# Optimization experiments

Measured on AMD Instinct MI355X. Metric: run time of the kernel, lower is better.

## Reference

```python
import jax, jax.numpy as jnp
import numpy as np

B, T, A = 4096, 32, 3
HID, D, N, K = 1024, 128, 16, 4096
FLAT = T * A            # 96
LAT = N * D             # 2048
COMMIT = 0.25


def setup_inputs() -> dict:
    key = jax.random.key(0)
    ks = jax.random.split(key, 14)
    s = 0.02
    return {
        "actions": jax.random.normal(ks[0], (B, T, A), jnp.float32),
        # encoder: FLAT -> HID -> HID -> N*D
        "e_w1": jax.random.normal(ks[1], (FLAT, HID), jnp.float32) * s,
        "e_b1": jnp.zeros((HID,), jnp.float32),
        "e_w2": jax.random.normal(ks[2], (HID, HID), jnp.float32) * s,
        "e_b2": jnp.zeros((HID,), jnp.float32),
        "e_w3": jax.random.normal(ks[3], (HID, LAT), jnp.float32) * s,
        "e_b3": jnp.zeros((LAT,), jnp.float32),
        # codebook init: uniform(-1/K, 1/K) as in torch init
        "codebook": jax.random.uniform(ks[4], (K, D), jnp.float32, -1.0 / K, 1.0 / K),
        # decoder: N*D -> HID -> HID -> FLAT
        "d_w1": jax.random.normal(ks[5], (LAT, HID), jnp.float32) * s,
        "d_b1": jnp.zeros((HID,), jnp.float32),
        "d_w2": jax.random.normal(ks[6], (HID, HID), jnp.float32) * s,
        "d_b2": jnp.zeros((HID,), jnp.float32),
        "d_w3": jax.random.normal(ks[7], (HID, FLAT), jnp.float32) * s,
        "d_b3": jnp.zeros((FLAT,), jnp.float32),
    }


def reference(actions, e_w1, e_b1, e_w2, e_b2, e_w3, e_b3, codebook,
              d_w1, d_b1, d_w2, d_b2, d_w3, d_b3):
    sg = jax.lax.stop_gradient
    b = actions.shape[0]
    # encode: [B, T*A] -> [B, N, D]
    flat = actions.reshape(b, FLAT)
    h = jax.nn.silu(flat @ e_w1 + e_b1)
    h = jax.nn.silu(h @ e_w2 + e_b2)
    latents = (h @ e_w3 + e_b3).reshape(b, N, D)
    # nearest-code search: [B*N, K] squared distances
    fl = latents.reshape(b * N, D)
    dist = (fl * fl).sum(1, keepdims=True) + (codebook * codebook).sum(1)[None, :] - 2.0 * (fl @ codebook.T)
    indices = jnp.argmin(dist, axis=1).reshape(b, N)
    quantized = codebook[indices]                      # [B, N, D]
    codebook_loss = jnp.mean((quantized - sg(latents)) ** 2)
    commitment_loss = jnp.mean((latents - sg(quantized)) ** 2)
    vq_loss = codebook_loss + COMMIT * commitment_loss
    q_st = latents + sg(quantized - latents)           # straight-through
    # decode
    g = jax.nn.silu(q_st.reshape(b, LAT) @ d_w1 + d_b1)
    g = jax.nn.silu(g @ d_w2 + d_b2)
    recon = (g @ d_w3 + d_b3).reshape(b, T, A)
    recon_loss = jnp.mean((recon - actions) ** 2)
    loss = recon_loss + vq_loss
    return recon, indices, vq_loss, recon_loss, loss
```

## Files before the change

kernel.cpp:

```cpp
#include <hip/hip_runtime.h>
#include <hip/hip_bf16.h>

#define DD 128

typedef float f2v __attribute__((ext_vector_type(2)));

__global__ void plant_diag(float val, float* out) {
    if (threadIdx.x == 0 && blockIdx.x == 0) out[0] = val;
}

__global__ void zero_acc(double* acc) {
    if (threadIdx.x == 0 && blockIdx.x == 0) { acc[0] = 0.0; acc[1] = 0.0; }
}

__device__ __forceinline__ float silu_np(float x) {
    float e = (float)exp(-(double)x);
    float u = 1.0f + e;
    float v = 1.0f / u;
    return x * v;
}

template <bool SILU>
__global__ __launch_bounds__(256) void gemm_db(const float* __restrict__ A,
                                               const float* __restrict__ W,
                                               const float* __restrict__ bias,
                                               float* __restrict__ C,
                                               int M, int N, int K) {
    __shared__ __align__(16) float As[128][36];
    __shared__ __align__(16) float Ws[32][68];
    const int t = threadIdx.x;
    const int tx = t & 15, ty = t >> 4;
    const int bm = blockIdx.y * 128, bn = blockIdx.x * 64;

    float acc[8][4];
#pragma unroll
    for (int i = 0; i < 8; ++i)
#pragma unroll
        for (int j = 0; j < 4; ++j) acc[i][j] = 0.0f;

    const int nPanels = (K + 31) / 32;
    float ra[16], rw[8];

    {
        const int k0 = 0;
#pragma unroll
        for (int it = 0; it < 16; ++it) {
            int e = t + 256 * it;
            int m = e >> 5, kk = e & 31;
            int mm = bm + m; if (mm >= M) mm = M - 1;
            int kc = k0 + kk;
            ra[it] = (kc < K) ? A[(size_t)mm * K + kc] : 0.0f;
        }
#pragma unroll
        for (int it = 0; it < 8; ++it) {
            int e = t + 256 * it;
            int r = e >> 6, c = e & 63;
            int n = bn + c;
            int kr = k0 + r;
            rw[it] = (kr < K && n < N) ? W[(size_t)kr * N + n] : 0.0f;
        }
    }

    for (int p = 0; p < nPanels; ++p) {
        __syncthreads();
#pragma unroll
        for (int it = 0; it < 16; ++it) {
            int e = t + 256 * it;
            As[e >> 5][e & 31] = ra[it];
        }
#pragma unroll
        for (int it = 0; it < 8; ++it) {
            int e = t + 256 * it;
            Ws[e >> 6][e & 63] = rw[it];
        }
        __syncthreads();

        if (p + 1 < nPanels) {
            const int k0 = (p + 1) * 32;
#pragma unroll
            for (int it = 0; it < 16; ++it) {
                int e = t + 256 * it;
                int m = e >> 5, kk = e & 31;
                int mm = bm + m; if (mm >= M) mm = M - 1;
                int kc = k0 + kk;
                ra[it] = (kc < K) ? A[(size_t)mm * K + kc] : 0.0f;
            }
#pragma unroll
            for (int it = 0; it < 8; ++it) {
                int e = t + 256 * it;
                int r = e >> 6, c = e & 63;
                int n = bn + c;
                int kr = k0 + r;
                rw[it] = (kr < K && n < N) ? W[(size_t)kr * N + n] : 0.0f;
            }
        }

#pragma unroll
        for (int kq = 0; kq < 8; ++kq) {
            float4 a4[8], w4[4];
#pragma unroll
            for (int i = 0; i < 8; ++i)
                a4[i] = *(const float4*)&As[ty + 16 * i][4 * kq];
#pragma unroll
            for (int q = 0; q < 4; ++q)
                w4[q] = *(const float4*)&Ws[4 * kq + q][4 * tx];
#pragma unroll
            for (int q = 0; q < 4; ++q) {
                const float wv[4] = {w4[q].x, w4[q].y, w4[q].z, w4[q].w};
#pragma unroll
                for (int i = 0; i < 8; ++i) {
                    const float av = ((const float*)&a4[i])[q];
#pragma unroll
                    for (int j = 0; j < 4; ++j)
                        acc[i][j] = fmaf(av, wv[j], acc[i][j]);
                }
            }
        }
    }

#pragma unroll
    for (int i = 0; i < 8; ++i) {
        int m = bm + ty + 16 * i;
#pragma unroll
        for (int j = 0; j < 4; ++j) {
            int n = bn + 4 * tx + j;
            if (m < M && n < N) {
                float x = acc[i][j] + bias[n];
                if (SILU) x = silu_np(x);
                C[(size_t)m * N + n] = x;
            }
        }
    }
}

__device__ __forceinline__ float pairwise128_sq(const float* __restrict__ x, int stride) {
    float r0 = x[0*stride]*x[0*stride], r1 = x[1*stride]*x[1*stride],
          r2 = x[2*stride]*x[2*stride], r3 = x[3*stride]*x[3*stride],
          r4 = x[4*stride]*x[4*stride], r5 = x[5*stride]*x[5*stride],
          r6 = x[6*stride]*x[6*stride], r7 = x[7*stride]*x[7*stride];
    for (int i = 8; i < 128; i += 8) {
        r0 += x[(i+0)*stride]*x[(i+0)*stride];
        r1 += x[(i+1)*stride]*x[(i+1)*stride];
        r2 += x[(i+2)*stride]*x[(i+2)*stride];
        r3 += x[(i+3)*stride]*x[(i+3)*stride];
        r4 += x[(i+4)*stride]*x[(i+4)*stride];
        r5 += x[(i+5)*stride]*x[(i+5)*stride];
        r6 += x[(i+6)*stride]*x[(i+6)*stride];
        r7 += x[(i+7)*stride]*x[(i+7)*stride];
    }
    return ((r0 + r1) + (r2 + r3)) + ((r4 + r5) + (r6 + r7));
}

__global__ void code_t2(const float* __restrict__ cb, float* __restrict__ t2, int K) {
    int k = blockIdx.x * 256 + threadIdx.x;
    if (k >= K) return;
    t2[k] = pairwise128_sq(cb + (size_t)k * DD, 1);
}

__global__ void cb_pack(const float* __restrict__ cb, float* __restrict__ cbP, int total) {
    int gid = blockIdx.x * 256 + threadIdx.x;
    if (gid >= total) return;
    int pair = gid >> 8;
    int r = gid & 255;
    int d = r >> 1, w = r & 1;
    cbP[gid] = cb[(size_t)(2 * pair + w) * DD + d];
}

#define VQG_ROWS 128
#define VQG_CPP  256
#define VQG_LT   132

__global__ __launch_bounds__(512) void vq_g88p(const float* __restrict__ lat,
                                               const float* __restrict__ cbP,
                                               const float* __restrict__ t2,
                                               float* __restrict__ pbv,
                                               int* __restrict__ pbk,
                                               int K, int rows_total) {
    __shared__ __align__(16) float Ls[VQG_ROWS][VQG_LT];
    __shared__ float T1s[VQG_ROWS];
    __shared__ float bwv[8][VQG_ROWS];
    __shared__ int   bwk[8][VQG_ROWS];

    const int t = threadIdx.x;
    const int tx = t & 15, ty = t >> 4;
    const int wave = t >> 6, lane = t & 63;
    const int r0 = blockIdx.x * VQG_ROWS;

#pragma unroll
    for (int it = 0; it < 8; ++it) {
        int g = t + 512 * it;
        int r = g >> 5, dq = g & 31;
        int rr = r0 + r; if (rr >= rows_total) rr = rows_total - 1;
        const float4 lv = *(const float4*)(lat + (size_t)rr * DD + 4 * dq);
        *(float4*)&Ls[r][4 * dq] = lv;
    }
    __syncthreads();

    if (t < VQG_ROWS) {
        const float* xr = &Ls[t][0];
        float4 q0 = *(const float4*)&xr[0];
        float4 q1 = *(const float4*)&xr[4];
        float a0 = q0.x*q0.x, a1 = q0.y*q0.y, a2 = q0.z*q0.z, a3 = q0.w*q0.w;
        float a4 = q1.x*q1.x, a5 = q1.y*q1.y, a6 = q1.z*q1.z, a7 = q1.w*q1.w;
#pragma unroll
        for (int i = 1; i < 16; ++i) {
            q0 = *(const float4*)&xr[8 * i];
            q1 = *(const float4*)&xr[8 * i + 4];
            a0 += q0.x*q0.x; a1 += q0.y*q0.y; a2 += q0.z*q0.z; a3 += q0.w*q0.w;
            a4 += q1.x*q1.x; a5 += q1.y*q1.y; a6 += q1.z*q1.z; a7 += q1.w*q1.w;
        }
        T1s[t] = ((a0 + a1) + (a2 + a3)) + ((a4 + a5) + (a6 + a7));
    }
    __syncthreads();

    float t1r[8];
#pragma unroll
    for (int i = 0; i < 8; ++i) t1r[i] = T1s[tx + 16 * i];

    float bestv[8]; int bestk[8];
#pragma unroll
    for (int i = 0; i < 8; ++i) { bestv[i] = 3.4e38f; bestk[i] = 0; }

    const int NP = K / VQG_CPP;
#pragma unroll 1
    for (int p = 0; p < NP; ++p) {
        const int kp = p * VQG_CPP;
        const int cbase = kp + 8 * ty;
        const float* cp0 = cbP + (size_t)cbase * DD;
        float t2v[8];
#pragma unroll
        for (int j = 0; j < 8; ++j) t2v[j] = t2[cbase + j];

        f2v s2[8][4];
#pragma unroll
        for (int i = 0; i < 8; ++i)
#pragma unroll
            for (int m = 0; m < 4; ++m) s2[i][m] = (f2v)(0.0f);

#pragma unroll 4
        for (int dq = 0; dq < 32; ++dq) {
            float4 u0[4], u1[4];
#pragma unroll
            for (int m = 0; m < 4; ++m) {
                u0[m] = *(const float4*)(cp0 + m * 256 + 8 * dq);
                u1[m] = *(const float4*)(cp0 + m * 256 + 8 * dq + 4);
            }
#pragma unroll
            for (int i = 0; i < 8; ++i) {
                const float4 la = *(const float4*)&Ls[tx + 16 * i][4 * dq];
                const f2v lx = {la.x, la.x}, ly = {la.y, la.y};
                const f2v lz = {la.z, la.z}, lw = {la.w, la.w};
#pragma unroll
                for (int m = 0; m < 4; ++m) {
                    const f2v c0 = {u0[m].x, u0[m].y};
                    const f2v c1 = {u0[m].z, u0[m].w};
                    const f2v c2 = {u1[m].x, u1[m].y};
                    const f2v c3 = {u1[m].z, u1[m].w};
                    s2[i][m] = __builtin_elementwise_fma(lx, c0, s2[i][m]);
                    s2[i][m] = __builtin_elementwise_fma(ly, c1, s2[i][m]);
                    s2[i][m] = __builtin_elementwise_fma(lz, c2, s2[i][m]);
                    s2[i][m] = __builtin_elementwise_fma(lw, c3, s2[i][m]);
                }
            }
        }

#pragma unroll
        for (int i = 0; i < 8; ++i) {
            const float tt1 = t1r[i];
#pragma unroll
            for (int m = 0; m < 4; ++m) {
                const int c0 = cbase + 2 * m;
                const float d0 = (tt1 + t2v[2 * m + 0]) - 2.0f * s2[i][m].x;
                const float d1 = (tt1 + t2v[2 * m + 1]) - 2.0f * s2[i][m].y;
                if (d0 < bestv[i]) { bestv[i] = d0; bestk[i] = c0; }
                if (d1 < bestv[i]) { bestv[i] = d1; bestk[i] = c0 + 1; }
            }
        }
    }

#pragma unroll
    for (int off = 16; off <= 32; off <<= 1) {
#pragma unroll
        for (int i = 0; i < 8; ++i) {
            float vv = __shfl_xor(bestv[i], off);
            int kk = __shfl_xor(bestk[i], off);
            if (vv < bestv[i] || (vv == bestv[i] && kk < bestk[i])) {
                bestv[i] = vv; bestk[i] = kk;
            }
        }
    }
    if (lane < 16) {
#pragma unroll
        for (int i = 0; i < 8; ++i) {
            bwv[wave][tx + 16 * i] = bestv[i];
            bwk[wave][tx + 16 * i] = bestk[i];
        }
    }
    __syncthreads();
    if (t < VQG_ROWS) {
        float bv = bwv[0][t]; int bk = bwk[0][t];
#pragma unroll
        for (int w = 1; w < 8; ++w) {
            float v = bwv[w][t]; int k = bwk[w][t];
            if (v < bv || (v == bv && k < bk)) { bv = v; bk = k; }
        }
        if (r0 + t < rows_total) {
            pbv[r0 + t] = bv;
            pbk[r0 + t] = bk;
        }
    }
}

__global__ __launch_bounds__(512) void vq_np4(const float* __restrict__ lat,
                                              const float* __restrict__ cb,
                                              const float* __restrict__ t2,
                                              float* __restrict__ pbv,
                                              int* __restrict__ pbk,
                                              int K, int Kc, int rows_total) {
    __shared__ __align__(16) float Ls[128][68];
    __shared__ __align__(16) float Cs[128][68];
    __shared__ float T1s[64];
    __shared__ float T2s[64];
    __shared__ float bwv[8][68];
    __shared__ int   bwk[8][68];

    const int t = threadIdx.x;
    const int tx = t & 15, ty = t >> 4;
    const int wave = t >> 6, lane = t & 63;
    const int r0 = blockIdx.x * 64;
    const int kbeg = blockIdx.y * Kc;
    const int kend = kbeg + Kc;

#pragma unroll
    for (int it = 0; it < 4; ++it) {
        int g = t + 512 * it;
        int row = g >> 5, dq = g & 31;
        int rr = r0 + row; if (rr >= rows_total) rr = rows_total - 1;
        const float4 v = *(const float4*)(lat + (size_t)rr * DD + 4 * dq);
        Ls[4*dq+0][row] = v.x; Ls[4*dq+1][row] = v.y;
        Ls[4*dq+2][row] = v.z; Ls[4*dq+3][row] = v.w;
    }
    __syncthreads();
    if (t < 64) T1s[t] = pairwise128_sq(&Ls[0][t], 68);

    float bestv[4]; int bestk[4];
#pragma unroll
    for (int r = 0; r < 4; ++r) { bestv[r] = 3.4e38f; bestk[r] = 0; }

    float4 pc[4];
    float pt2 = 0.0f;
#pragma unroll
    for (int it = 0; it < 4; ++it) {
        int g = t + 512 * it;
        int c = g >> 5, dq = g & 31;
        int cc = kbeg + c; if (cc >= K) cc = K - 1;
        pc[it] = *(const float4*)(cb + (size_t)cc * DD + 4 * dq);
    }
    if (t < 64) { int cc = kbeg + t; if (cc >= K) cc = K - 1; pt2 = t2[cc]; }

    for (int k0 = kbeg; k0 < kend; k0 += 64) {
        __syncthreads();
#pragma unroll
        for (int it = 0; it < 4; ++it) {
            int g = t + 512 * it;
            int c = g >> 5, dq = g & 31;
            Cs[4*dq+0][c] = pc[it].x; Cs[4*dq+1][c] = pc[it].y;
            Cs[4*dq+2][c] = pc[it].z; Cs[4*dq+3][c] = pc[it].w;
        }
        if (t < 64) T2s[t] = pt2;
        __syncthreads();

        if (k0 + 64 < kend) {
            const int kn = k0 + 64;
#pragma unroll
            for (int it = 0; it < 4; ++it) {
                int g = t + 512 * it;
                int c = g >> 5, dq = g & 31;
                int cc = kn + c; if (cc >= K) cc = K - 1;
                pc[it] = *(const float4*)(cb + (size_t)cc * DD + 4 * dq);
            }
            if (t < 64) { int cc = kn + t; if (cc >= K) cc = K - 1; pt2 = t2[cc]; }
        }

        float s[4][2];
#pragma unroll
        for (int r = 0; r < 4; ++r) { s[r][0] = 0.0f; s[r][1] = 0.0f; }

#pragma unroll 8
        for (int d = 0; d < 128; ++d) {
            const float4 a4 = *(const float4*)&Ls[d][4 * tx];
            const float2 c2 = *(const float2*)&Cs[d][2 * ty];
            const float av[4] = {a4.x, a4.y, a4.z, a4.w};
#pragma unroll
            for (int r = 0; r < 4; ++r) {
                s[r][0] = fmaf(av[r], c2.x, s[r][0]);
                s[r][1] = fmaf(av[r], c2.y, s[r][1]);
            }
        }

#pragma unroll
        for (int r = 0; r < 4; ++r) {
            const float t1 = T1s[4 * tx + r];
#pragma unroll
            for (int j = 0; j < 2; ++j) {
                int kc = k0 + 2 * ty + j;
                float dist = (t1 + T2s[2 * ty + j]) - 2.0f * s[r][j];
                if (kc < K && dist < bestv[r]) { bestv[r] = dist; bestk[r] = kc; }
            }
        }
    }

#pragma unroll
    for (int off = 16; off <= 32; off <<= 1) {
#pragma unroll
        for (int r = 0; r < 4; ++r) {
            float vv = __shfl_xor(bestv[r], off);
            int kk = __shfl_xor(bestk[r], off);
            if (vv < bestv[r] || (vv == bestv[r] && kk < bestk[r])) {
                bestv[r] = vv; bestk[r] = kk;
            }
        }
    }
    if (lane < 16) {
#pragma unroll
        for (int r = 0; r < 4; ++r) {
            bwv[wave][4 * lane + r] = bestv[r];
            bwk[wave][4 * lane + r] = bestk[r];
        }
    }
    __syncthreads();
    if (t < 64) {
        float bv = bwv[0][t]; int bk = bwk[0][t];
#pragma unroll
        for (int w = 1; w < 8; ++w) {
            float v = bwv[w][t]; int k = bwk[w][t];
            if (v < bv || (v == bv && k < bk)) { bv = v; bk = k; }
        }
        if (r0 + t < rows_total) {
            size_t o = (size_t)blockIdx.y * rows_total + (r0 + t);
            pbv[o] = bv;
            pbk[o] = bk;
        }
    }
}

__global__ __launch_bounds__(256) void vq_combine(const float* __restrict__ pbv,
                                                  const int* __restrict__ pbk,
                                                  int S, int rows,
                                                  int* __restrict__ indices,
                                                  double* __restrict__ acc) {
    int r = blockIdx.x * 256 + threadIdx.x;
    float bv = 3.4e38f; int bk = 0;
    if (r < rows) {
        for (int s = 0; s < S; ++s) {
            float v = pbv[(size_t)s * rows + r];
            int k = pbk[(size_t)s * rows + r];
            if (v < bv) { bv = v; bk = k; }
        }
        indices[r] = bk;
    }
    __shared__ double red[256];
    red[threadIdx.x] = (r < rows) ? (double)bv : 0.0;
    __syncthreads();
    for (int s = 128; s > 0; s >>= 1) {
        if (threadIdx.x < s) red[threadIdx.x] += red[threadIdx.x + s];
        __syncthreads();
    }
    if (threadIdx.x == 0) atomicAdd(acc, red[0]);
}

__global__ void q_gather(const int* __restrict__ idx, const float* __restrict__ cb,
                         float* __restrict__ Q, int count, int nlat) {
    int gid = blockIdx.x * 256 + threadIdx.x;
    if (gid >= count) return;
    int m = gid >> 11;
    int j = gid & 2047;
    int code = idx[m * nlat + (j >> 7)];
    Q[gid] = cb[((size_t)code << 7) + (j & 127)];
}

__global__ __launch_bounds__(256) void recon_out(const float* __restrict__ recon,
                                                 const float* __restrict__ actions,
                                                 float* __restrict__ out,
                                                 double* __restrict__ acc, int count) {
    int gid = blockIdx.x * 256 + threadIdx.x;
    double sq = 0.0;
    if (gid < count) {
        float rv = recon[gid];
        float av = actions[gid];
        double diff = (double)rv - (double)av;
        out[gid] = rv;
        sq = diff * diff;
    }
    __shared__ double red[256];
    red[threadIdx.x] = sq;
    __syncthreads();
    for (int s = 128; s > 0; s >>= 1) {
        if (threadIdx.x < s) red[threadIdx.x] += red[threadIdx.x + s];
        __syncthreads();
    }
    if (threadIdx.x == 0) atomicAdd(acc + 1, red[0]);
}

__global__ void idx_out(const int* __restrict__ idx, float* __restrict__ out, int count) {
    int gid = blockIdx.x * 256 + threadIdx.x;
    if (gid < count) out[gid] = (float)idx[gid];
}

__global__ void finalize(const double* __restrict__ acc, float* __restrict__ out,
                         double vq_den, double rec_den) {
    double vq = 1.25 * acc[0] / vq_den;
    double rl = acc[1] / rec_den;
    out[0] = (float)vq;
    out[1] = (float)rl;
    out[2] = (float)(rl + vq);
}

static inline int ceildiv(int a, int b) { return (a + b - 1) / b; }

extern "C" void kernel_launch(void* const* d_in, const int* in_sizes, int n_in,
                              void* d_out, int out_size, void* d_ws, size_t ws_size,
                              hipStream_t stream) {
    const float* actions = (const float*)d_in[0];
    const float* e_w1 = (const float*)d_in[1];
    const float* e_b1 = (const float*)d_in[2];
    const float* e_w2 = (const float*)d_in[3];
    const float* e_b2 = (const float*)d_in[4];
    const float* e_w3 = (const float*)d_in[5];
    const float* e_b3 = (const float*)d_in[6];
    const float* cb   = (const float*)d_in[7];
    const float* d_w1 = (const float*)d_in[8];
    const float* d_b1 = (const float*)d_in[9];
    const float* d_w2 = (const float*)d_in[10];
    const float* d_b2 = (const float*)d_in[11];
    const float* d_w3 = (const float*)d_in[12];
    const float* d_b3 = (const float*)d_in[13];
    float* out = (float*)d_out;

    const int FLAT = in_sizes[13];
    const int B    = in_sizes[0] / FLAT;
    const int HID  = in_sizes[2];
    const int LAT  = in_sizes[6];
    const int K    = in_sizes[7] / DD;
    const int NL   = LAT / DD;

    const bool g88 = (K % VQG_CPP == 0);
    const int S = 1;
    const int Kc = K;

    int CHUNK = B;
    auto need = [&](int ch) -> size_t {
        return (size_t)ch * HID * 4 * 2 + (size_t)ch * LAT * 4 * 2
             + (size_t)ch * HID * 4 * 2 + (size_t)ch * FLAT * 4
             + (size_t)K * 4 + (size_t)K * DD * 4 + 64 + (size_t)B * NL * 4
             + (size_t)ch * NL * S * 8;
    };
    while (CHUNK > 16 && need(CHUNK) > ws_size) CHUNK >>= 1;
    if (need(CHUNK) > ws_size) {
        plant_diag<<<1, 64, 0, stream>>>(2222.0f, out);
        return;
    }
    const int NCHUNK = ceildiv(B, CHUNK);

    char* ws = (char*)d_ws;
    size_t off = 0;
    float* h1c  = (float*)(ws + off); off += (size_t)CHUNK * HID * 4;
    float* h2c  = (float*)(ws + off); off += (size_t)CHUNK * HID * 4;
    float* latc = (float*)(ws + off); off += (size_t)CHUNK * LAT * 4;
    float* Qc   = (float*)(ws + off); off += (size_t)CHUNK * LAT * 4;
    float* g1c  = (float*)(ws + off); off += (size_t)CHUNK * HID * 4;
    float* g2c  = (float*)(ws + off); off += (size_t)CHUNK * HID * 4;
    float* recc = (float*)(ws + off); off += (size_t)CHUNK * FLAT * 4;
    float* t2   = (float*)(ws + off); off += (size_t)K * 4;
    float* cbP  = (float*)(ws + off); off += (size_t)K * DD * 4;
    double* acc = (double*)(ws + off); off += 64;
    int*   idx  = (int*)(ws + off);   off += (size_t)B * NL * 4;
    float* pbv  = (float*)(ws + off); off += (size_t)CHUNK * NL * S * 4;
    int*   pbk  = (int*)(ws + off);

    zero_acc<<<1, 64, 0, stream>>>(acc);
    code_t2<<<ceildiv(K, 256), 256, 0, stream>>>(cb, t2, K);
    if (g88) {
        cb_pack<<<ceildiv(K * DD, 256), 256, 0, stream>>>(cb, cbP, K * DD);
    }

    for (int c = 0; c < NCHUNK; ++c) {
        const int r0 = c * CHUNK;
        const int cbR = (B - r0 < CHUNK) ? (B - r0) : CHUNK;
        const float* act_c = actions + (size_t)r0 * FLAT;
        int* idx_c = idx + (size_t)r0 * NL;
        const int rows = cbR * NL;

        gemm_db<true><<<dim3(ceildiv(HID, 64), ceildiv(cbR, 128)), 256, 0, stream>>>(
            act_c, e_w1, e_b1, h1c, cbR, HID, FLAT);
        gemm_db<true><<<dim3(ceildiv(HID, 64), ceildiv(cbR, 128)), 256, 0, stream>>>(
            h1c, e_w2, e_b2, h2c, cbR, HID, HID);
        gemm_db<false><<<dim3(ceildiv(LAT, 64), ceildiv(cbR, 128)), 256, 0, stream>>>(
            h2c, e_w3, e_b3, latc, cbR, LAT, HID);

        if (g88) {
            vq_g88p<<<ceildiv(rows, VQG_ROWS), 512, 0, stream>>>(
                latc, cbP, t2, pbv, pbk, K, rows);
        } else {
            vq_np4<<<dim3(ceildiv(rows, 64), S), 512, 0, stream>>>(
                latc, cb, t2, pbv, pbk, K, Kc, rows);
        }
        vq_combine<<<ceildiv(rows, 256), 256, 0, stream>>>(pbv, pbk, S, rows, idx_c, acc);

        q_gather<<<ceildiv(cbR * LAT, 256), 256, 0, stream>>>(idx_c, cb, Qc, cbR * LAT, NL);
        gemm_db<true><<<dim3(ceildiv(HID, 64), ceildiv(cbR, 128)), 256, 0, stream>>>(
            Qc, d_w1, d_b1, g1c, cbR, HID, LAT);
        gemm_db<true><<<dim3(ceildiv(HID, 64), ceildiv(cbR, 128)), 256, 0, stream>>>(
            g1c, d_w2, d_b2, g2c, cbR, HID, HID);
        gemm_db<false><<<dim3(ceildiv(FLAT, 64), ceildiv(cbR, 128)), 256, 0, stream>>>(
            g2c, d_w3, d_b3, recc, cbR, FLAT, HID);

        recon_out<<<ceildiv(cbR * FLAT, 256), 256, 0, stream>>>(
            recc, act_c, out + (size_t)r0 * FLAT, acc, cbR * FLAT);
    }

    idx_out<<<ceildiv(B * NL, 256), 256, 0, stream>>>(idx, out + (size_t)B * FLAT, B * NL);
    finalize<<<1, 1, 0, stream>>>(acc, out + (size_t)B * FLAT + (size_t)B * NL,
                                  (double)B * NL * DD, (double)B * FLAT);
}
```

Measured before the change: 1.778 ms.

## Pre-pack weights into panel layout and read W directly from global memory in GEMM

```diff
diff --git a/kernel.cpp b/kernel.cpp
--- a/kernel.cpp
+++ b/kernel.cpp
@@ -18,6 +18,112 @@
     float u = 1.0f + e;
     float v = 1.0f / u;
     return x * v;
+}
+
+__global__ void w_pack(const float* __restrict__ W, float* __restrict__ Wp,
+                       int K, int N, int K32, int total) {
+    int gid = blockIdx.x * 256 + threadIdx.x;
+    if (gid >= total) return;
+    int c = gid & 63;
+    int k = (gid >> 6) % K32;
+    int pn = gid / (K32 * 64);
+    int n = pn * 64 + c;
+    Wp[gid] = (k < K && n < N) ? W[(size_t)k * N + n] : 0.0f;
+}
+
+template <bool SILU>
+__global__ __launch_bounds__(256) void gemm_wp(const float* __restrict__ A,
+                                               const float* __restrict__ Wp,
+                                               const float* __restrict__ bias,
+                                               float* __restrict__ C,
+                                               int M, int N, int K) {
+    __shared__ __align__(16) float As[128][36];
+    const int t = threadIdx.x;
+    const int tx = t & 15, ty = t >> 4;
+    const int bm = blockIdx.y * 128, bn = blockIdx.x * 64;
+    const int K32 = ((K + 31) / 32) * 32;
+
+    float acc[8][4];
+#pragma unroll
+    for (int i = 0; i < 8; ++i)
+#pragma unroll
+        for (int j = 0; j < 4; ++j) acc[i][j] = 0.0f;
+
+    const int nPanels = (K + 31) / 32;
+    float ra[16];
+
+    {
+        const int k0 = 0;
+#pragma unroll
+        for (int it = 0; it < 16; ++it) {
+            int e = t + 256 * it;
+            int m = e >> 5, kk = e & 31;
+            int mm = bm + m; if (mm >= M) mm = M - 1;
+            int kc = k0 + kk;
+            ra[it] = (kc < K) ? A[(size_t)mm * K + kc] : 0.0f;
+        }
+    }
+
+    const float* wpc = Wp + (size_t)blockIdx.x * K32 * 64 + 4 * tx + 1024;
+
+    for (int p = 0; p < nPanels; ++p) {
+        __syncthreads();
+#pragma unroll
+        for (int it = 0; it < 16; ++it) {
+            int e = t + 256 * it;
+            As[e >> 5][e & 31] = ra[it];
+        }
+        __syncthreads();
+
+        if (p + 1 < nPanels) {
+            const int k0 = (p + 1) * 32;
+#pragma unroll
+            for (int it = 0; it < 16; ++it) {
+                int e = t + 256 * it;
+                int m = e >> 5, kk = e & 31;
+                int mm = bm + m; if (mm >= M) mm = M - 1;
+                int kc = k0 + kk;
+                ra[it] = (kc < K) ? A[(size_t)mm * K + kc] : 0.0f;
+            }
+        }
+
+        const float* wq = wpc + (size_t)p * 2048;
+#pragma unroll
+        for (int kq = 0; kq < 8; ++kq) {
+            float4 a4[8], w4[4];
+#pragma unroll
+            for (int i = 0; i < 8; ++i)
+                a4[i] = *(const float4*)&As[ty + 16 * i][4 * kq];
+#pragma unroll
+            for (int q = 0; q < 4; ++q)
+                w4[q] = *(const float4*)(wq + (4 * kq + q) * 64 - 1024);
+#pragma unroll
+            for (int q = 0; q < 4; ++q) {
+                const float wv[4] = {w4[q].x, w4[q].y, w4[q].z, w4[q].w};
+#pragma unroll
+                for (int i = 0; i < 8; ++i) {
+                    const float av = ((const float*)&a4[i])[q];
+#pragma unroll
+                    for (int j = 0; j < 4; ++j)
+                        acc[i][j] = fmaf(av, wv[j], acc[i][j]);
+                }
+            }
+        }
+    }
+
+#pragma unroll
+    for (int i = 0; i < 8; ++i) {
+        int m = bm + ty + 16 * i;
+#pragma unroll
+        for (int j = 0; j < 4; ++j) {
+            int n = bn + 4 * tx + j;
+            if (m < M && n < N) {
+                float x = acc[i][j] + bias[n];
+                if (SILU) x = silu_np(x);
+                C[(size_t)m * N + n] = x;
+            }
+        }
+    }
 }
 
 template <bool SILU>
@@ -548,15 +654,30 @@
     const int S = 1;
     const int Kc = K;
 
+    const float* wsrc[6] = {e_w1, e_w2, e_w3, d_w1, d_w2, d_w3};
+    const int wK[6] = {FLAT, HID, HID, LAT, HID, HID};
+    const int wN[6] = {HID, HID, LAT, HID, HID, FLAT};
+    size_t wpOff[6];
+    size_t wpTot = 0;
+    for (int i = 0; i < 6; ++i) {
+        int K32 = ceildiv(wK[i], 32) * 32;
+        int Pn = ceildiv(wN[i], 64);
+        wpOff[i] = wpTot;
+        wpTot += (size_t)Pn * K32 * 64;
+    }
+
     int CHUNK = B;
-    auto need = [&](int ch) -> size_t {
+    bool useWp = true;
+    auto need = [&](int ch, bool wp) -> size_t {
         return (size_t)ch * HID * 4 * 2 + (size_t)ch * LAT * 4 * 2
              + (size_t)ch * HID * 4 * 2 + (size_t)ch * FLAT * 4
-             + (size_t)K * 4 + (size_t)K * DD * 4 + 64 + (size_t)B * NL * 4
+             + (size_t)K * 4 + (size_t)K * DD * 4 + (wp ? wpTot * 4 : 0)
+             + 64 + (size_t)B * NL * 4
              + (size_t)ch * NL * S * 8;
     };
-    while (CHUNK > 16 && need(CHUNK) > ws_size) CHUNK >>= 1;
-    if (need(CHUNK) > ws_size) {
+    if (need(B, true) > ws_size) useWp = false;
+    while (CHUNK > 16 && need(CHUNK, useWp) > ws_size) CHUNK >>= 1;
+    if (need(CHUNK, useWp) > ws_size) {
         plant_diag<<<1, 64, 0, stream>>>(2222.0f, out);
         return;
     }
@@ -573,6 +694,7 @@
     float* recc = (float*)(ws + off); off += (size_t)CHUNK * FLAT * 4;
     float* t2   = (float*)(ws + off); off += (size_t)K * 4;
     float* cbP  = (float*)(ws + off); off += (size_t)K * DD * 4;
+    float* Wp   = (float*)(ws + off); off += useWp ? wpTot * 4 : 0;
     double* acc = (double*)(ws + off); off += 64;
     int*   idx  = (int*)(ws + off);   off += (size_t)B * NL * 4;
     float* pbv  = (float*)(ws + off); off += (size_t)CHUNK * NL * S * 4;
@@ -583,6 +705,27 @@
     if (g88) {
         cb_pack<<<ceildiv(K * DD, 256), 256, 0, stream>>>(cb, cbP, K * DD);
     }
+    if (useWp) {
+        for (int i = 0; i < 6; ++i) {
+            int K32 = ceildiv(wK[i], 32) * 32;
+            int Pn = ceildiv(wN[i], 64);
+            int total = Pn * K32 * 64;
+            w_pack<<<ceildiv(total, 256), 256, 0, stream>>>(
+                wsrc[i], Wp + wpOff[i], wK[i], wN[i], K32, total);
+        }
+    }
+
+    auto GEMM = [&](int li, bool silu, const float* Araw, const float* bias, float* Cout,
+                    int M, int N, int Kd) {
+        dim3 grid(ceildiv(N, 64), ceildiv(M, 128));
+        if (useWp) {
+            if (silu) gemm_wp<true><<<grid, 256, 0, stream>>>(Araw, Wp + wpOff[li], bias, Cout, M, N, Kd);
+            else      gemm_wp<false><<<grid, 256, 0, stream>>>(Araw, Wp + wpOff[li], bias, Cout, M, N, Kd);
+        } else {
+            if (silu) gemm_db<true><<<grid, 256, 0, stream>>>(Araw, wsrc[li], bias, Cout, M, N, Kd);
+            else      gemm_db<false><<<grid, 256, 0, stream>>>(Araw, wsrc[li], bias, Cout, M, N, Kd);
+        }
+    };
 
     for (int c = 0; c < NCHUNK; ++c) {
         const int r0 = c * CHUNK;
@@ -591,12 +734,9 @@
         int* idx_c = idx + (size_t)r0 * NL;
         const int rows = cbR * NL;
 
-        gemm_db<true><<<dim3(ceildiv(HID, 64), ceildiv(cbR, 128)), 256, 0, stream>>>(
-            act_c, e_w1, e_b1, h1c, cbR, HID, FLAT);
-        gemm_db<true><<<dim3(ceildiv(HID, 64), ceildiv(cbR, 128)), 256, 0, stream>>>(
-            h1c, e_w2, e_b2, h2c, cbR, HID, HID);
-        gemm_db<false><<<dim3(ceildiv(LAT, 64), ceildiv(cbR, 128)), 256, 0, stream>>>(
-            h2c, e_w3, e_b3, latc, cbR, LAT, HID);
+        GEMM(0, true,  act_c, e_b1, h1c, cbR, HID, FLAT);
+        GEMM(1, true,  h1c,   e_b2, h2c, cbR, HID, HID);
+        GEMM(2, false, h2c,   e_b3, latc, cbR, LAT, HID);
 
         if (g88) {
             vq_g88p<<<ceildiv(rows, VQG_ROWS), 512, 0, stream>>>(
@@ -608,12 +748,9 @@
         vq_combine<<<ceildiv(rows, 256), 256, 0, stream>>>(pbv, pbk, S, rows, idx_c, acc);
 
         q_gather<<<ceildiv(cbR * LAT, 256), 256, 0, stream>>>(idx_c, cb, Qc, cbR * LAT, NL);
-        gemm_db<true><<<dim3(ceildiv(HID, 64), ceildiv(cbR, 128)), 256, 0, stream>>>(
-            Qc, d_w1, d_b1, g1c, cbR, HID, LAT);
-        gemm_db<true><<<dim3(ceildiv(HID, 64), ceildiv(cbR, 128)), 256, 0, stream>>>(
-            g1c, d_w2, d_b2, g2c, cbR, HID, HID);
-        gemm_db<false><<<dim3(ceildiv(FLAT, 64), ceildiv(cbR, 128)), 256, 0, stream>>>(
-            g2c, d_w3, d_b3, recc, cbR, FLAT, HID);
+        GEMM(3, true,  Qc,  d_b1, g1c, cbR, HID, LAT);
+        GEMM(4, true,  g1c, d_b2, g2c, cbR, HID, HID);
+        GEMM(5, false, g2c, d_b3, recc, cbR, FLAT, HID);
 
         recon_out<<<ceildiv(cbR * FLAT, 256), 256, 0, stream>>>(
             recc, act_c, out + (size_t)r0 * FLAT, acc, cbR * FLAT);
```

Result: slower. 1.907 ms (+7.3%).
